# Optimization experiments

Hardware: AMD Instinct MI355X
Metric: run time of the kernel (lower is better)

## Reference

```python
import jax, jax.numpy as jnp
import numpy as np

EPS = 1e-6


def _ln_linear(W, x):
    # W: [out_ch, in_ch]; x: [B, in_ch, K, N] -> [B, out_ch, K, N]
    return jnp.einsum('of,bfkn->bokn', W, x)


def _killing_relu_so3(D, x):
    # x: [B, F, 3, N]. so3 Killing form K(a,b) = tr(a_hat b_hat) = -2 a.b (negative definite).
    d = jnp.einsum('gf,bfkn->bgkn', D, x)              # learned direction per channel
    k_xd = -2.0 * jnp.sum(x * d, axis=2, keepdims=True)
    k_dd = -2.0 * jnp.sum(d * d, axis=2, keepdims=True)  # <= 0
    # LN-ReLU: keep x where K(x,d) < 0 (i.e. <x,d> > 0), else remove Killing projection onto d
    return jnp.where(k_xd < 0.0, x, x - (k_xd / (k_dd - EPS)) * d)


def _map_m(W, D, z):
    # z: [1, 20, 3, 1] -> LNLinearAndKillingRelu(20, 3) -> rearrange '1 f k 1 -> k f' = [3,3]
    y = _killing_relu_so3(D, _ln_linear(W, z))
    return y[0, :, :, 0].T


def _bracket_mix(Wb, z, Ma, Mb):
    # LNLinearAndLieBracketChannelMix with residual_connect=True, so3 bracket = cross product
    y = _ln_linear(Wb, z)                      # [B, 20, 3, 1]
    y1 = jnp.einsum('ij,bfjn->bfin', Ma, y)    # mix algebra (K) dim with 3x3 M
    y2 = jnp.einsum('ij,bfjn->bfin', Mb, y)
    br = jnp.cross(y1, y2, axis=2)             # so3 Lie bracket
    return br + y                              # residual connection


def _interp_u(t, u, Dt):
    # faithful jit-safe version of interpolate_u
    T = u.shape[0]
    ii = jnp.clip(jnp.floor(t / Dt).astype(jnp.int32), 0, T - 1)
    u_i = u[ii]
    u_n = u[jnp.minimum(ii + 1, T - 1)]
    frac = (t - ii.astype(t.dtype) * Dt) / Dt
    return jnp.where(ii >= T - 1, u_i, u_i + frac * (u_n - u_i))


def setup_inputs() -> dict:
    key = jax.random.key(0)
    ks = jax.random.split(key, 16)
    B, T, F = 524288, 16, 20
    s = 1.0 / np.sqrt(F)
    s3 = 1.0 / np.sqrt(3.0)
    inp = {
        't': jax.random.uniform(ks[0], (1,), jnp.float32),
        'x': jax.random.normal(ks[1], (B, 1, 3), jnp.float32),
        'u': jax.random.normal(ks[2], (T, B, 1, 3), jnp.float32),
        'Dt': 1,
        'R': jax.random.normal(ks[3], (3, 3), jnp.float32),
        'm': 0.1 * jax.random.normal(ks[4], (3, F), jnp.float32),
        'W1': s * jax.random.normal(ks[5], (3, F), jnp.float32),
        'W2': s * jax.random.normal(ks[6], (3, F), jnp.float32),
        'W3': s * jax.random.normal(ks[7], (3, F), jnp.float32),
        'W4': s * jax.random.normal(ks[8], (3, F), jnp.float32),
        'D1': s3 * jax.random.normal(ks[9], (3, 3), jnp.float32),
        'D2': s3 * jax.random.normal(ks[10], (3, 3), jnp.float32),
        'D3': s3 * jax.random.normal(ks[11], (3, 3), jnp.float32),
        'D4': s3 * jax.random.normal(ks[12], (3, 3), jnp.float32),
        'Wb1': jax.random.normal(ks[13], (F, 1), jnp.float32),
        'Wb2': jax.random.normal(ks[14], (F, 1), jnp.float32),
        'Wout': s * jax.random.normal(ks[15], (1, F), jnp.float32),
    }
    return inp


def reference(t, x, u, Dt, R, m, W1, W2, W3, W4, D1, D2, D3, D4, Wb1, Wb2, Wout):
    ts = t[0]
    ut = _interp_u(ts, u, Dt)                 # [B, 1, 3]
    x_r = x[..., None]                        # [B, 1, 3, 1]
    u_r = ut[..., None]
    base = (R @ m).T[None, :, :, None]        # 'k f -> 1 f k 1' : [1, 20, 3, 1]
    m1 = _map_m(W1, D1, base)
    m2 = _map_m(W2, D2, base)
    m3 = _map_m(W3, D3, base)
    m4 = _map_m(W4, D4, base)
    M1 = m1 @ m1.T
    M2 = m2 @ m2.T
    M3 = m3 @ m3.T
    M4 = m4 @ m4.T
    x_out = _bracket_mix(Wb1, x_r, M1, M2)    # [B, 20, 3, 1]
    u_out = _bracket_mix(Wb2, u_r, M3, M4)
    out = _ln_linear(Wout, x_out + u_out)     # [B, 1, 3, 1]
    return out[..., 0]                        # 'b f d 1 -> b f d'
```

## Files before the change

### kernel.cpp

```cpp
#include <hip/hip_runtime.h>
#include <math.h>

#define EPS_K 1e-6f

__global__ void setup_kernel(
    const float* __restrict__ t, const int* __restrict__ Dt,
    const float* __restrict__ R, const float* __restrict__ m,
    const float* __restrict__ W1, const float* __restrict__ W2,
    const float* __restrict__ W3, const float* __restrict__ W4,
    const float* __restrict__ D1, const float* __restrict__ D2,
    const float* __restrict__ D3, const float* __restrict__ D4,
    const float* __restrict__ Wb1, const float* __restrict__ Wb2,
    const float* __restrict__ Wout,
    float* __restrict__ ws, int F, int T)
{
    __shared__ float sbase[3][64];
    __shared__ float sy[4][3][3];
    __shared__ float syo[4][3][3];
    const int tid = threadIdx.x;

    for (int idx = tid; idx < 3 * F; idx += blockDim.x) {
        int k = idx / F, f = idx - k * F;
        sbase[k][f] = R[k*3+0]*m[0*F+f] + R[k*3+1]*m[1*F+f] + R[k*3+2]*m[2*F+f];
    }
    __syncthreads();

    const float* Ws[4] = {W1, W2, W3, W4};
    const float* Ds[4] = {D1, D2, D3, D4};

    if (tid < 36) {
        int mp = tid / 9, r = tid - mp * 9;
        int g = r / 3, k = r - g * 3;
        const float* W = Ws[mp];
        float acc = 0.f;
        for (int f = 0; f < F; ++f) acc += W[g*F + f] * sbase[k][f];
        sy[mp][g][k] = acc;
    }
    __syncthreads();

    if (tid < 12) {
        int mp = tid / 3, g = tid - mp * 3;
        const float* D = Ds[mp];
        float d0 = 0.f, d1 = 0.f, d2 = 0.f;
        for (int f = 0; f < 3; ++f) {
            float w = D[g*3 + f];
            d0 += w * sy[mp][f][0];
            d1 += w * sy[mp][f][1];
            d2 += w * sy[mp][f][2];
        }
        float y0 = sy[mp][g][0], y1 = sy[mp][g][1], y2 = sy[mp][g][2];
        float kxd = -2.f * (y0*d0 + y1*d1 + y2*d2);
        float kdd = -2.f * (d0*d0 + d1*d1 + d2*d2);
        if (kxd < 0.f) {
            syo[mp][g][0] = y0; syo[mp][g][1] = y1; syo[mp][g][2] = y2;
        } else {
            float s = kxd / (kdd - EPS_K);
            syo[mp][g][0] = y0 - s*d0; syo[mp][g][1] = y1 - s*d1; syo[mp][g][2] = y2 - s*d2;
        }
    }
    __syncthreads();

    if (tid < 36) {
        int mp = tid / 9, r = tid - mp * 9;
        int a = r / 3, b = r - a * 3;
        float acc = 0.f;
        for (int g = 0; g < 3; ++g) acc += syo[mp][g][a] * syo[mp][g][b];
        ws[mp*9 + a*3 + b] = acc;
    } else if (tid < 40) {
        int c = tid - 36;
        const float* Wb = (c < 2) ? Wb1 : Wb2;
        const bool sq = (c == 0) || (c == 2);
        float acc = 0.f;
        for (int f = 0; f < F; ++f) {
            float w = Wb[f];
            acc += Wout[f] * (sq ? w*w : w);
        }
        ws[36 + c] = acc;
    } else if (tid == 40) {
        float ts = t[0];
        float Df = (float)Dt[0];
        int ii = (int)floorf(ts / Df);
        if (ii < 0) ii = 0;
        if (ii > T - 1) ii = T - 1;
        float frac = (ts - (float)ii * Df) / Df;
        int ia = ii;
        int ib = (ii + 1 > T - 1) ? (T - 1) : (ii + 1);
        float frac_eff = (ii >= T - 1) ? 0.f : frac;
        ws[40] = frac_eff;
        ((int*)ws)[41] = ia;
        ((int*)ws)[42] = ib;
    }
}

__device__ __forceinline__ void elem_compute(
    const float* __restrict__ M,
    float c1, float c2, float c3, float c4,
    float x0, float x1, float x2,
    float u0, float u1, float u2,
    float& o0, float& o1, float& o2)
{
    const float* M1 = M;      const float* M2 = M + 9;
    const float* M3 = M + 18; const float* M4 = M + 27;
    float p0 = M1[0]*x0 + M1[1]*x1 + M1[2]*x2;
    float p1 = M1[3]*x0 + M1[4]*x1 + M1[5]*x2;
    float p2 = M1[6]*x0 + M1[7]*x1 + M1[8]*x2;
    float q0 = M2[0]*x0 + M2[1]*x1 + M2[2]*x2;
    float q1 = M2[3]*x0 + M2[4]*x1 + M2[5]*x2;
    float q2 = M2[6]*x0 + M2[7]*x1 + M2[8]*x2;
    float cx0 = p1*q2 - p2*q1;
    float cx1 = p2*q0 - p0*q2;
    float cx2 = p0*q1 - p1*q0;
    float r0 = M3[0]*u0 + M3[1]*u1 + M3[2]*u2;
    float r1 = M3[3]*u0 + M3[4]*u1 + M3[5]*u2;
    float r2 = M3[6]*u0 + M3[7]*u1 + M3[8]*u2;
    float s0 = M4[0]*u0 + M4[1]*u1 + M4[2]*u2;
    float s1 = M4[3]*u0 + M4[4]*u1 + M4[5]*u2;
    float s2 = M4[6]*u0 + M4[7]*u1 + M4[8]*u2;
    float cu0 = r1*s2 - r2*s1;
    float cu1 = r2*s0 - r0*s2;
    float cu2 = r0*s1 - r1*s0;
    o0 = c1*cx0 + c2*x0 + c3*cu0 + c4*u0;
    o1 = c1*cx1 + c2*x1 + c3*cu1 + c4*u1;
    o2 = c1*cx2 + c2*x2 + c3*cu2 + c4*u2;
}

__global__ void __launch_bounds__(256) lnode_main(
    const float* __restrict__ x, const float* __restrict__ u,
    const float* __restrict__ ws, float* __restrict__ out, int B)
{
    __shared__ float s[41];
    __shared__ int si[2];
    const int tid = threadIdx.x;
    if (tid < 41) s[tid] = ws[tid];
    if (tid < 2)  si[tid] = ((const int*)ws)[41 + tid];
    __syncthreads();

    float M[36];
#pragma unroll
    for (int i = 0; i < 36; ++i) M[i] = s[i];
    const float c1 = s[36], c2 = s[37], c3 = s[38], c4 = s[39];
    const float frac = s[40];
    const float* __restrict__ ua = u + (size_t)si[0] * (size_t)B * 3u;
    const float* __restrict__ ub = u + (size_t)si[1] * (size_t)B * 3u;

    const long long gidx = (long long)blockIdx.x * blockDim.x + tid;

    if ((B & 3) == 0) {
        const long long nq = (long long)(B >> 2);
        if (gidx >= nq) return;
        const float4* __restrict__ x4 = (const float4*)x;
        const float4* __restrict__ a4 = (const float4*)ua;
        const float4* __restrict__ b4 = (const float4*)ub;
        float4* __restrict__ o4 = (float4*)out;

        float4 X[3], A[3], Bv[3];
#pragma unroll
        for (int i = 0; i < 3; ++i) {
            X[i]  = x4[gidx*3 + i];
            A[i]  = a4[gidx*3 + i];
            Bv[i] = b4[gidx*3 + i];
        }
        float xf[12], uf[12], of[12];
#pragma unroll
        for (int i = 0; i < 3; ++i) {
            xf[i*4+0] = X[i].x; xf[i*4+1] = X[i].y; xf[i*4+2] = X[i].z; xf[i*4+3] = X[i].w;
            uf[i*4+0] = A[i].x + frac * (Bv[i].x - A[i].x);
            uf[i*4+1] = A[i].y + frac * (Bv[i].y - A[i].y);
            uf[i*4+2] = A[i].z + frac * (Bv[i].z - A[i].z);
            uf[i*4+3] = A[i].w + frac * (Bv[i].w - A[i].w);
        }
#pragma unroll
        for (int e = 0; e < 4; ++e) {
            elem_compute(M, c1, c2, c3, c4,
                         xf[e*3+0], xf[e*3+1], xf[e*3+2],
                         uf[e*3+0], uf[e*3+1], uf[e*3+2],
                         of[e*3+0], of[e*3+1], of[e*3+2]);
        }
#pragma unroll
        for (int i = 0; i < 3; ++i) {
            o4[gidx*3 + i] = make_float4(of[i*4+0], of[i*4+1], of[i*4+2], of[i*4+3]);
        }
    } else {
        if (gidx >= B) return;
        const size_t o = (size_t)gidx * 3u;
        float x0 = x[o+0], x1 = x[o+1], x2 = x[o+2];
        float u0 = ua[o+0] + frac * (ub[o+0] - ua[o+0]);
        float u1 = ua[o+1] + frac * (ub[o+1] - ua[o+1]);
        float u2 = ua[o+2] + frac * (ub[o+2] - ua[o+2]);
        float o0, o1, o2;
        elem_compute(M, c1, c2, c3, c4, x0, x1, x2, u0, u1, u2, o0, o1, o2);
        out[o+0] = o0; out[o+1] = o1; out[o+2] = o2;
    }
}

extern "C" void kernel_launch(void* const* d_in, const int* in_sizes, int n_in,
                              void* d_out, int out_size, void* d_ws, size_t ws_size,
                              hipStream_t stream)
{
    const float* t    = (const float*)d_in[0];
    const float* x    = (const float*)d_in[1];
    const float* u    = (const float*)d_in[2];
    const int*   Dt   = (const int*)d_in[3];
    const float* R    = (const float*)d_in[4];
    const float* m    = (const float*)d_in[5];
    const float* W1   = (const float*)d_in[6];
    const float* W2   = (const float*)d_in[7];
    const float* W3   = (const float*)d_in[8];
    const float* W4   = (const float*)d_in[9];
    const float* D1   = (const float*)d_in[10];
    const float* D2   = (const float*)d_in[11];
    const float* D3   = (const float*)d_in[12];
    const float* D4   = (const float*)d_in[13];
    const float* Wb1  = (const float*)d_in[14];
    const float* Wb2  = (const float*)d_in[15];
    const float* Wout = (const float*)d_in[16];
    float* out = (float*)d_out;
    float* ws  = (float*)d_ws;

    const int B = in_sizes[1] / 3;
    const int T = in_sizes[2] / in_sizes[1];
    const int F = in_sizes[5] / 3;

    setup_kernel<<<1, 64, 0, stream>>>(t, Dt, R, m, W1, W2, W3, W4,
                                       D1, D2, D3, D4, Wb1, Wb2, Wout, ws, F, T);

    const long long n = ((B & 3) == 0) ? (long long)B / 4 : (long long)B;
    const int blocks = (int)((n + 255) / 256);
    lnode_main<<<blocks, 256, 0, stream>>>(x, u, ws, out, B);
}
```

Before: 14.10 us.

## Fuse setup kernel into main kernel, recomputing constants per block

Removes the single-block setup kernel launch and its dependency. Each block now recomputes the tiny 3x3 matrices and mixing coefficients in shared memory, and issues its streaming loads of x and u before that setup so the global-load latency overlaps the setup arithmetic. Output stores become nontemporal. The cost is redundant setup work in every block, three extra block barriers, and the vector registers held live across that setup.

Measured after the change: 13.62 us. 3.4% less time.

```diff
diff --git a/kernel.cpp b/kernel.cpp
--- a/kernel.cpp
+++ b/kernel.cpp
@@ -3,94 +3,8 @@
 
 #define EPS_K 1e-6f
 
-__global__ void setup_kernel(
-    const float* __restrict__ t, const int* __restrict__ Dt,
-    const float* __restrict__ R, const float* __restrict__ m,
-    const float* __restrict__ W1, const float* __restrict__ W2,
-    const float* __restrict__ W3, const float* __restrict__ W4,
-    const float* __restrict__ D1, const float* __restrict__ D2,
-    const float* __restrict__ D3, const float* __restrict__ D4,
-    const float* __restrict__ Wb1, const float* __restrict__ Wb2,
-    const float* __restrict__ Wout,
-    float* __restrict__ ws, int F, int T)
-{
-    __shared__ float sbase[3][64];
-    __shared__ float sy[4][3][3];
-    __shared__ float syo[4][3][3];
-    const int tid = threadIdx.x;
-
-    for (int idx = tid; idx < 3 * F; idx += blockDim.x) {
-        int k = idx / F, f = idx - k * F;
-        sbase[k][f] = R[k*3+0]*m[0*F+f] + R[k*3+1]*m[1*F+f] + R[k*3+2]*m[2*F+f];
-    }
-    __syncthreads();
-
-    const float* Ws[4] = {W1, W2, W3, W4};
-    const float* Ds[4] = {D1, D2, D3, D4};
-
-    if (tid < 36) {
-        int mp = tid / 9, r = tid - mp * 9;
-        int g = r / 3, k = r - g * 3;
-        const float* W = Ws[mp];
-        float acc = 0.f;
-        for (int f = 0; f < F; ++f) acc += W[g*F + f] * sbase[k][f];
-        sy[mp][g][k] = acc;
-    }
-    __syncthreads();
-
-    if (tid < 12) {
-        int mp = tid / 3, g = tid - mp * 3;
-        const float* D = Ds[mp];
-        float d0 = 0.f, d1 = 0.f, d2 = 0.f;
-        for (int f = 0; f < 3; ++f) {
-            float w = D[g*3 + f];
-            d0 += w * sy[mp][f][0];
-            d1 += w * sy[mp][f][1];
-            d2 += w * sy[mp][f][2];
-        }
-        float y0 = sy[mp][g][0], y1 = sy[mp][g][1], y2 = sy[mp][g][2];
-        float kxd = -2.f * (y0*d0 + y1*d1 + y2*d2);
-        float kdd = -2.f * (d0*d0 + d1*d1 + d2*d2);
-        if (kxd < 0.f) {
-            syo[mp][g][0] = y0; syo[mp][g][1] = y1; syo[mp][g][2] = y2;
-        } else {
-            float s = kxd / (kdd - EPS_K);
-            syo[mp][g][0] = y0 - s*d0; syo[mp][g][1] = y1 - s*d1; syo[mp][g][2] = y2 - s*d2;
-        }
-    }
-    __syncthreads();
-
-    if (tid < 36) {
-        int mp = tid / 9, r = tid - mp * 9;
-        int a = r / 3, b = r - a * 3;
-        float acc = 0.f;
-        for (int g = 0; g < 3; ++g) acc += syo[mp][g][a] * syo[mp][g][b];
-        ws[mp*9 + a*3 + b] = acc;
-    } else if (tid < 40) {
-        int c = tid - 36;
-        const float* Wb = (c < 2) ? Wb1 : Wb2;
-        const bool sq = (c == 0) || (c == 2);
-        float acc = 0.f;
-        for (int f = 0; f < F; ++f) {
-            float w = Wb[f];
-            acc += Wout[f] * (sq ? w*w : w);
-        }
-        ws[36 + c] = acc;
-    } else if (tid == 40) {
-        float ts = t[0];
-        float Df = (float)Dt[0];
-        int ii = (int)floorf(ts / Df);
-        if (ii < 0) ii = 0;
-        if (ii > T - 1) ii = T - 1;
-        float frac = (ts - (float)ii * Df) / Df;
-        int ia = ii;
-        int ib = (ii + 1 > T - 1) ? (T - 1) : (ii + 1);
-        float frac_eff = (ii >= T - 1) ? 0.f : frac;
-        ws[40] = frac_eff;
-        ((int*)ws)[41] = ia;
-        ((int*)ws)[42] = ib;
-    }
-}
+typedef float f32x4 __attribute__((ext_vector_type(4)));
+
 
 __device__ __forceinline__ void elem_compute(
     const float* __restrict__ M,
@@ -124,42 +38,133 @@
     o2 = c1*cx2 + c2*x2 + c3*cu2 + c4*u2;
 }
 
-__global__ void __launch_bounds__(256) lnode_main(
+__global__ void __launch_bounds__(256) lnode_fused(
+    const float* __restrict__ t, const int* __restrict__ Dt,
     const float* __restrict__ x, const float* __restrict__ u,
-    const float* __restrict__ ws, float* __restrict__ out, int B)
+    const float* __restrict__ R, const float* __restrict__ m,
+    const float* __restrict__ W1, const float* __restrict__ W2,
+    const float* __restrict__ W3, const float* __restrict__ W4,
+    const float* __restrict__ D1, const float* __restrict__ D2,
+    const float* __restrict__ D3, const float* __restrict__ D4,
+    const float* __restrict__ Wb1, const float* __restrict__ Wb2,
+    const float* __restrict__ Wout,
+    float* __restrict__ out, int B, int T, int F)
 {
-    __shared__ float s[41];
-    __shared__ int si[2];
+    __shared__ float sbase[3][64];
+    __shared__ float sy[4][3][3];
+    __shared__ float syo[4][3][3];
+    __shared__ float sC[40];
     const int tid = threadIdx.x;
-    if (tid < 41) s[tid] = ws[tid];
-    if (tid < 2)  si[tid] = ((const int*)ws)[41 + tid];
-    __syncthreads();
+
+    const float ts  = t[0];
+    const float Dtf = (float)Dt[0];
+    int ii = (int)floorf(ts / Dtf);
+    ii = ii < 0 ? 0 : (ii > T - 1 ? T - 1 : ii);
+    const float frac = (ii >= T - 1) ? 0.f : (ts - (float)ii * Dtf) / Dtf;
+    const int ibn = (ii + 1 > T - 1) ? (T - 1) : (ii + 1);
+
+    const float* __restrict__ ua = u + (size_t)ii  * (size_t)B * 3u;
+    const float* __restrict__ ub = u + (size_t)ibn * (size_t)B * 3u;
+
+    const long long gidx = (long long)blockIdx.x * blockDim.x + tid;
+    const bool vec = ((B & 3) == 0);
+
+    f32x4 X[3], A[3], Bv[3];
+    float sx0=0, sx1=0, sx2=0, su0=0, su1=0, su2=0;
+    bool active;
+    if (vec) {
+        const long long nq = (long long)(B >> 2);
+        active = gidx < nq;
+        if (active) {
+            const f32x4* __restrict__ x4 = (const f32x4*)x;
+            const f32x4* __restrict__ a4 = (const f32x4*)ua;
+            const f32x4* __restrict__ b4 = (const f32x4*)ub;
+#pragma unroll
+            for (int i = 0; i < 3; ++i) {
+                X[i]  = x4[gidx*3 + i];
+                A[i]  = a4[gidx*3 + i];
+                Bv[i] = b4[gidx*3 + i];
+            }
+        }
+    } else {
+        active = gidx < B;
+        if (active) {
+            const size_t o = (size_t)gidx * 3u;
+            sx0 = x[o+0]; sx1 = x[o+1]; sx2 = x[o+2];
+            float a0 = ua[o+0], a1 = ua[o+1], a2 = ua[o+2];
+            float b0 = ub[o+0], b1 = ub[o+1], b2 = ub[o+2];
+            su0 = a0 + frac*(b0-a0); su1 = a1 + frac*(b1-a1); su2 = a2 + frac*(b2-a2);
+        }
+    }
+
+    for (int idx = tid; idx < 3 * F; idx += blockDim.x) {
+        int k = idx / F, f = idx - k * F;
+        sbase[k][f] = R[k*3+0]*m[0*F+f] + R[k*3+1]*m[1*F+f] + R[k*3+2]*m[2*F+f];
+    }
+    __syncthreads();
+
+    const float* Ws[4] = {W1, W2, W3, W4};
+    const float* Ds[4] = {D1, D2, D3, D4};
+
+    if (tid < 36) {
+        int mp = tid / 9, r = tid - mp * 9;
+        int g = r / 3, k = r - g * 3;
+        const float* W = Ws[mp];
+        float acc = 0.f;
+        for (int f = 0; f < F; ++f) acc += W[g*F + f] * sbase[k][f];
+        sy[mp][g][k] = acc;
+    }
+    __syncthreads();
+
+    if (tid < 12) {
+        int mp = tid / 3, g = tid - mp * 3;
+        const float* D = Ds[mp];
+        float d0 = 0.f, d1 = 0.f, d2 = 0.f;
+        for (int f = 0; f < 3; ++f) {
+            float w = D[g*3 + f];
+            d0 += w * sy[mp][f][0];
+            d1 += w * sy[mp][f][1];
+            d2 += w * sy[mp][f][2];
+        }
+        float y0 = sy[mp][g][0], y1 = sy[mp][g][1], y2 = sy[mp][g][2];
+        float kxd = -2.f * (y0*d0 + y1*d1 + y2*d2);
+        float kdd = -2.f * (d0*d0 + d1*d1 + d2*d2);
+        if (kxd < 0.f) {
+            syo[mp][g][0] = y0; syo[mp][g][1] = y1; syo[mp][g][2] = y2;
+        } else {
+            float s = kxd / (kdd - EPS_K);
+            syo[mp][g][0] = y0 - s*d0; syo[mp][g][1] = y1 - s*d1; syo[mp][g][2] = y2 - s*d2;
+        }
+    }
+    __syncthreads();
+
+    if (tid < 36) {
+        int mp = tid / 9, r = tid - mp * 9;
+        int a = r / 3, b = r - a * 3;
+        float acc = 0.f;
+        for (int g = 0; g < 3; ++g) acc += syo[mp][g][a] * syo[mp][g][b];
+        sC[mp*9 + a*3 + b] = acc;
+    } else if (tid < 40) {
+        int c = tid - 36;
+        const float* Wb = (c < 2) ? Wb1 : Wb2;
+        const bool sq = (c == 0) || (c == 2);
+        float acc = 0.f;
+        for (int f = 0; f < F; ++f) {
+            float w = Wb[f];
+            acc += Wout[f] * (sq ? w*w : w);
+        }
+        sC[36 + c] = acc;
+    }
+    __syncthreads();
+
+    if (!active) return;
 
     float M[36];
 #pragma unroll
-    for (int i = 0; i < 36; ++i) M[i] = s[i];
-    const float c1 = s[36], c2 = s[37], c3 = s[38], c4 = s[39];
-    const float frac = s[40];
-    const float* __restrict__ ua = u + (size_t)si[0] * (size_t)B * 3u;
-    const float* __restrict__ ub = u + (size_t)si[1] * (size_t)B * 3u;
-
-    const long long gidx = (long long)blockIdx.x * blockDim.x + tid;
-
-    if ((B & 3) == 0) {
-        const long long nq = (long long)(B >> 2);
-        if (gidx >= nq) return;
-        const float4* __restrict__ x4 = (const float4*)x;
-        const float4* __restrict__ a4 = (const float4*)ua;
-        const float4* __restrict__ b4 = (const float4*)ub;
-        float4* __restrict__ o4 = (float4*)out;
-
-        float4 X[3], A[3], Bv[3];
-#pragma unroll
-        for (int i = 0; i < 3; ++i) {
-            X[i]  = x4[gidx*3 + i];
-            A[i]  = a4[gidx*3 + i];
-            Bv[i] = b4[gidx*3 + i];
-        }
+    for (int i = 0; i < 36; ++i) M[i] = sC[i];
+    const float c1 = sC[36], c2 = sC[37], c3 = sC[38], c4 = sC[39];
+
+    if (vec) {
         float xf[12], uf[12], of[12];
 #pragma unroll
         for (int i = 0; i < 3; ++i) {
@@ -176,19 +181,17 @@
                          uf[e*3+0], uf[e*3+1], uf[e*3+2],
                          of[e*3+0], of[e*3+1], of[e*3+2]);
         }
+        f32x4* __restrict__ o4 = (f32x4*)out;
 #pragma unroll
         for (int i = 0; i < 3; ++i) {
-            o4[gidx*3 + i] = make_float4(of[i*4+0], of[i*4+1], of[i*4+2], of[i*4+3]);
+            f32x4 v;
+            v.x = of[i*4+0]; v.y = of[i*4+1]; v.z = of[i*4+2]; v.w = of[i*4+3];
+            __builtin_nontemporal_store(v, &o4[gidx*3 + i]);
         }
     } else {
-        if (gidx >= B) return;
+        float o0, o1, o2;
+        elem_compute(M, c1, c2, c3, c4, sx0, sx1, sx2, su0, su1, su2, o0, o1, o2);
         const size_t o = (size_t)gidx * 3u;
-        float x0 = x[o+0], x1 = x[o+1], x2 = x[o+2];
-        float u0 = ua[o+0] + frac * (ub[o+0] - ua[o+0]);
-        float u1 = ua[o+1] + frac * (ub[o+1] - ua[o+1]);
-        float u2 = ua[o+2] + frac * (ub[o+2] - ua[o+2]);
-        float o0, o1, o2;
-        elem_compute(M, c1, c2, c3, c4, x0, x1, x2, u0, u1, u2, o0, o1, o2);
         out[o+0] = o0; out[o+1] = o1; out[o+2] = o2;
     }
 }
@@ -215,16 +218,15 @@
     const float* Wb2  = (const float*)d_in[15];
     const float* Wout = (const float*)d_in[16];
     float* out = (float*)d_out;
-    float* ws  = (float*)d_ws;
 
     const int B = in_sizes[1] / 3;
     const int T = in_sizes[2] / in_sizes[1];
     const int F = in_sizes[5] / 3;
 
-    setup_kernel<<<1, 64, 0, stream>>>(t, Dt, R, m, W1, W2, W3, W4,
-                                       D1, D2, D3, D4, Wb1, Wb2, Wout, ws, F, T);
-
     const long long n = ((B & 3) == 0) ? (long long)B / 4 : (long long)B;
     const int blocks = (int)((n + 255) / 256);
-    lnode_main<<<blocks, 256, 0, stream>>>(x, u, ws, out, B);
+
+    lnode_fused<<<blocks, 256, 0, stream>>>(t, Dt, x, u, R, m,
+                                            W1, W2, W3, W4, D1, D2, D3, D4,
+                                            Wb1, Wb2, Wout, out, B, T, F);
 }
```
